# Kernel optimization log

Hardware: AMD Instinct MI355X
Metric: run time of the kernel (lower is better)

The kernel has to match this reference:

```python
import jax, jax.numpy as jnp
import numpy as np

IN_FEATURES = 3
CODE_NUM = 64
CODE_CHANNEL = 64
SHAPE_NUM = 1


def setup_inputs() -> dict:
    key = jax.random.key(0)
    k1, k2 = jax.random.split(key)
    coords = jax.random.uniform(k1, (8, 65536, IN_FEATURES), dtype=jnp.float32)  # in [0,1) subset of [-1,1]
    table_size = SHAPE_NUM * CODE_NUM ** IN_FEATURES
    # xavier_uniform for [C, N] matrix
    limit = float(np.sqrt(6.0 / (CODE_CHANNEL + table_size)))
    shape_code = jax.random.uniform(k2, (CODE_CHANNEL, table_size), dtype=jnp.float32,
                                    minval=-limit, maxval=limit)
    return {"coords": coords, "shape_code": shape_code, "idx": 0}


def reference(coords, shape_code, idx):
    D = IN_FEATURES
    # corner offset mask: [2^D, D] of {0,1}
    mask = jnp.stack(jnp.meshgrid(*([jnp.arange(2, dtype=jnp.float32)] * D), indexing="ij"), -1)
    mask = mask.reshape(-1, D)                                   # [8, 3]
    mul = jnp.asarray([CODE_NUM ** i for i in range(D)], dtype=jnp.int64)
    offset = jnp.asarray(idx, dtype=jnp.int64) * (CODE_NUM ** D)

    c = (coords + 1.0) * ((CODE_NUM - 1) / 2.0)                  # [B, P, 3] in [0, code_num-1]
    corners = jnp.floor(c)[..., None, :] + mask                  # [B, P, 8, 3]
    coordsf = c[..., None, :] - corners                          # [B, P, 8, 3]
    index = jnp.sum(corners.astype(jnp.int64) * mul, axis=-1) + offset  # [B, P, 8]
    weights = jnp.prod(1.0 - jnp.abs(coordsf), axis=-1)          # [B, P, 8]

    code = jnp.take(shape_code, index, axis=1)                   # [C, B, P, 8] gather
    out = jnp.einsum("cbpk,bpk->bpc", code, weights)             # weighted corner sum
    return out
```

## Files before the change

kernel.cpp:

```cpp
#include <hip/hip_runtime.h>


#define CODE_NUM 64
#define CODE_CHANNEL 64
#define TABLE (CODE_NUM * CODE_NUM * CODE_NUM)
#define NBINS 4096
#define SCAT_PTS 1024
#define SCAT_PPT 4
#define TBLOCKS (TABLE / 64)
#define LROW 68

typedef float f4_t __attribute__((ext_vector_type(4)));

__device__ __forceinline__ void nt_store_f4(float* p, float x, float y, float z, float w) {
    f4_t v = {x, y, z, w};
    __builtin_nontemporal_store(v, (f4_t*)p);
}

__global__ __launch_bounds__(256) void init_k(int* __restrict__ hist, int* __restrict__ bbox,
                                              int* __restrict__ done) {
    const int t = blockIdx.x * 256 + threadIdx.x;
    for (int i = t; i < NBINS; i += gridDim.x * 256) hist[i] = 0;
    if (t == 0) {
        bbox[0] = 0x7fffffff; bbox[1] = (int)0x80000000;
        bbox[2] = 0x7fffffff; bbox[3] = (int)0x80000000;
        done[0] = 0;
    }
}

__device__ __forceinline__ int cell_bin(float x, float y, float z,
                                        int& ix, int& iy, int& iz) {
    ix = (int)floorf((x + 1.0f) * ((CODE_NUM - 1) * 0.5f));
    iy = (int)floorf((y + 1.0f) * ((CODE_NUM - 1) * 0.5f));
    iz = (int)floorf((z + 1.0f) * ((CODE_NUM - 1) * 0.5f));
    const int cx = min(max(ix, 0), 63) >> 2;
    const int cy = min(max(iy, 0), 63) >> 2;
    const int cz = min(max(iz, 0), 63) >> 2;
    return cx | (cy << 4) | (cz << 8);
}

__global__ __launch_bounds__(256) void hist_scan_k(const float* __restrict__ coords, int npoints,
                                                   int* __restrict__ hist, int* __restrict__ bbox,
                                                   int* __restrict__ done,
                                                   int* __restrict__ cursor,
                                                   int* __restrict__ starts) {
    __shared__ int lh[NBINS];
    __shared__ int lb[4];
    __shared__ int lastflag;
    __shared__ int wbase[4];
    for (int i = threadIdx.x; i < NBINS; i += 256) lh[i] = 0;
    if (threadIdx.x == 0) {
        lb[0] = 0x7fffffff; lb[1] = (int)0x80000000;
        lb[2] = 0x7fffffff; lb[3] = (int)0x80000000;
        lastflag = 0;
    }
    __syncthreads();
    int ymin = 0x7fffffff, ymax = (int)0x80000000;
    int zmin = 0x7fffffff, zmax = (int)0x80000000;
    const int stride = gridDim.x * 256;
    for (int p = blockIdx.x * 256 + threadIdx.x; p < npoints; p += stride) {
        const float x = coords[p * 3 + 0];
        const float y = coords[p * 3 + 1];
        const float z = coords[p * 3 + 2];
        int ix, iy, iz;
        const int bin = cell_bin(x, y, z, ix, iy, iz);
        atomicAdd(&lh[bin], 1);
        ymin = min(ymin, iy); ymax = max(ymax, iy);
        zmin = min(zmin, iz); zmax = max(zmax, iz);
    }
    atomicMin(&lb[0], ymin); atomicMax(&lb[1], ymax);
    atomicMin(&lb[2], zmin); atomicMax(&lb[3], zmax);
    __syncthreads();
    for (int i = threadIdx.x; i < NBINS; i += 256) {
        const int c = lh[i];
        if (c) atomicAdd(&hist[i], c);
    }
    if (threadIdx.x == 0) {
        atomicMin(&bbox[0], lb[0]); atomicMax(&bbox[1], lb[1]);
        atomicMin(&bbox[2], lb[2]); atomicMax(&bbox[3], lb[3]);
    }
    __threadfence();
    __syncthreads();
    if (threadIdx.x == 0) {
        const int r = atomicAdd(done, 1);
        if (r == (int)gridDim.x - 1) lastflag = 1;
    }
    __syncthreads();
    if (!lastflag) return;

    const int t = threadIdx.x;
    int h[16];
    int s = 0;
#pragma unroll
    for (int j = 0; j < 16; ++j) {
        h[j] = atomicAdd(&hist[t * 16 + j], 0);
        s += h[j];
    }
    const int lane = t & 63, wv = t >> 6;
    int inc = s;
#pragma unroll
    for (int d = 1; d < 64; d <<= 1) {
        const int u = __shfl_up(inc, d, 64);
        if (lane >= d) inc += u;
    }
    if (lane == 63) wbase[wv] = inc;
    __syncthreads();
    int wex = 0;
#pragma unroll
    for (int w = 0; w < 4; ++w)
        if (w < wv) wex += wbase[w];
    int run = wex + (inc - s);
#pragma unroll
    for (int j = 0; j < 16; ++j) {
        cursor[t * 16 + j] = run;
        starts[t * 16 + j] = run;
        run += h[j];
    }
    if (t == 255) starts[NBINS] = npoints;
}

__global__ __launch_bounds__(256) void mid_fused_k(const float* __restrict__ src,
                                                   float* __restrict__ dst,
                                                   const int* __restrict__ bbox,
                                                   const float* __restrict__ coords, int npoints,
                                                   int* __restrict__ cursor,
                                                   float4* __restrict__ sorted) {
    __shared__ int smem[64 * 65];

    if (blockIdx.x < TBLOCKS) {
        const int t0 = blockIdx.x * 64;
        const int y = (t0 >> 6) & 63;
        const int z = t0 >> 12;
        if (y < bbox[0] || y > bbox[1] + 1 || z < bbox[2] || z > bbox[3] + 1) return;

        float* tile = (float*)smem;
        const int j = threadIdx.x;
#pragma unroll
        for (int i = 0; i < 4; ++i) {
            const int q = (i << 8) | j;
            const int c = q >> 4;
            const int tc4 = q & 15;
            const float4 v = *(const float4*)(src + (size_t)c * TABLE + t0 + (tc4 << 2));
            tile[((tc4 << 2) + 0) * 65 + c] = v.x;
            tile[((tc4 << 2) + 1) * 65 + c] = v.y;
            tile[((tc4 << 2) + 2) * 65 + c] = v.z;
            tile[((tc4 << 2) + 3) * 65 + c] = v.w;
        }
        __syncthreads();
#pragma unroll
        for (int i = 0; i < 4; ++i) {
            const int q = (i << 8) | j;
            const int t = q >> 4;
            const int c4 = q & 15;
            nt_store_f4(dst + (size_t)(t0 + t) * 64 + (c4 << 2),
                        tile[t * 65 + (c4 << 2) + 0],
                        tile[t * 65 + (c4 << 2) + 1],
                        tile[t * 65 + (c4 << 2) + 2],
                        tile[t * 65 + (c4 << 2) + 3]);
        }
    } else {
        int* lcount = smem;
        for (int i = threadIdx.x; i < NBINS; i += 256) lcount[i] = 0;
        __syncthreads();

        const int p0 = (int)(blockIdx.x - TBLOCKS) * SCAT_PTS;
        float px[SCAT_PPT], py[SCAT_PPT], pz[SCAT_PPT];
        int pbin[SCAT_PPT], prank[SCAT_PPT];

#pragma unroll
        for (int i = 0; i < SCAT_PPT; ++i) {
            const int p = p0 + (i << 8) + (int)threadIdx.x;
            pbin[i] = -1;
            if (p < npoints) {
                const float x = coords[p * 3 + 0];
                const float y = coords[p * 3 + 1];
                const float z = coords[p * 3 + 2];
                int ix, iy, iz;
                const int bin = cell_bin(x, y, z, ix, iy, iz);
                px[i] = x; py[i] = y; pz[i] = z;
                pbin[i] = bin;
                prank[i] = atomicAdd(&lcount[bin], 1);
            }
        }
        __syncthreads();

        for (int i = threadIdx.x; i < NBINS; i += 256) {
            const int c = lcount[i];
            if (c) lcount[i] = atomicAdd(&cursor[i], c);
        }
        __syncthreads();

#pragma unroll
        for (int i = 0; i < SCAT_PPT; ++i) {
            if (pbin[i] >= 0) {
                const int p = p0 + (i << 8) + (int)threadIdx.x;
                const int slot = lcount[pbin[i]] + prank[i];
                sorted[slot] = make_float4(px[i], py[i], pz[i], __int_as_float(p));
            }
        }
    }
}

__global__ __launch_bounds__(256) void interp_bin_k(const float4* __restrict__ sorted,
                                                    const float* __restrict__ table,
                                                    const int* __restrict__ starts,
                                                    float* __restrict__ out,
                                                    int npoints) {
    unsigned bid = blockIdx.x;
    bid = (bid & 7u) * (NBINS / 8) + (bid >> 3);
    const int s = starts[bid];
    const int e = starts[bid + 1];
    if (e <= s) return;

    const int x0 = (bid & 15) << 2;
    const int y0 = ((bid >> 4) & 15) << 2;
    const int z0 = (bid >> 8) << 2;

    __shared__ float lds[125 * LROW];

    const f4_t* tt4 = (const f4_t*)table;
    for (int i = threadIdx.x; i < 125 * 16; i += 256) {
        const int row = i >> 4, o = i & 15;
        const int dx = row % 5;
        const int seg = row / 5;
        const int dy = seg % 5, dz = seg / 5;
        const int cell = (z0 + dz) * (CODE_NUM * CODE_NUM) + (y0 + dy) * CODE_NUM + (x0 + dx);
        *(f4_t*)&lds[row * LROW + (o << 2)] = tt4[(size_t)cell * 16 + o];
    }
    __syncthreads();

    const int lane = threadIdx.x & 63;
    const int wv = threadIdx.x >> 6;
    const int sub = lane >> 4;
    const int cg = lane & 15;

    for (int p = s + wv * 4 + sub; p < e; p += 16) {
        const float4 s4 = sorted[p];
        const int op = __float_as_int(s4.w);

        const float sx = (s4.x + 1.0f) * ((CODE_NUM - 1) * 0.5f);
        const float sy = (s4.y + 1.0f) * ((CODE_NUM - 1) * 0.5f);
        const float sz = (s4.z + 1.0f) * ((CODE_NUM - 1) * 0.5f);
        const float fx = floorf(sx), fy = floorf(sy), fz = floorf(sz);
        const float rx = sx - fx, ry = sy - fy, rz = sz - fz;
        const int ix = (int)fx, iy = (int)fy, iz = (int)fz;
        const int r0 = ((iz - z0) * 5 + (iy - y0)) * 5 + (ix - x0);

        const float wx[2] = {1.0f - rx, rx};
        const float wy[2] = {1.0f - ry, ry};
        const float wz[2] = {1.0f - rz, rz};

        float4 acc = make_float4(0.f, 0.f, 0.f, 0.f);
#pragma unroll
        for (int k = 0; k < 8; ++k) {
            const int a = k & 1, b = (k >> 1) & 1, c = (k >> 2) & 1;
            const int row = r0 + a + 5 * b + 25 * c;
            const float w = wx[a] * wy[b] * wz[c];
            const float4 v = *(const float4*)&lds[row * LROW + (cg << 2)];
            acc.x = fmaf(w, v.x, acc.x);
            acc.y = fmaf(w, v.y, acc.y);
            acc.z = fmaf(w, v.z, acc.z);
            acc.w = fmaf(w, v.w, acc.w);
        }
        nt_store_f4(out + (size_t)op * CODE_CHANNEL + (cg << 2), acc.x, acc.y, acc.z, acc.w);
    }
}

__global__ __launch_bounds__(256) void transpose_k(const float* __restrict__ src,
                                                   float* __restrict__ dst) {
    __shared__ float tile[64 * 65];
    const int t0 = blockIdx.x * 64;
    const int j = threadIdx.x;
#pragma unroll
    for (int i = 0; i < 4; ++i) {
        const int q = (i << 8) | j;
        const int c = q >> 4;
        const int tc4 = q & 15;
        const float4 v = *(const float4*)(src + (size_t)c * TABLE + t0 + (tc4 << 2));
        tile[((tc4 << 2) + 0) * 65 + c] = v.x;
        tile[((tc4 << 2) + 1) * 65 + c] = v.y;
        tile[((tc4 << 2) + 2) * 65 + c] = v.z;
        tile[((tc4 << 2) + 3) * 65 + c] = v.w;
    }
    __syncthreads();
#pragma unroll
    for (int i = 0; i < 4; ++i) {
        const int q = (i << 8) | j;
        const int t = q >> 4;
        const int c4 = q & 15;
        float4 v;
        v.x = tile[t * 65 + (c4 << 2) + 0];
        v.y = tile[t * 65 + (c4 << 2) + 1];
        v.z = tile[t * 65 + (c4 << 2) + 2];
        v.w = tile[t * 65 + (c4 << 2) + 3];
        *(float4*)(dst + (size_t)(t0 + t) * 64 + (c4 << 2)) = v;
    }
}

__global__ __launch_bounds__(256) void interp4_k(const float* __restrict__ coords,
                                                 const float* __restrict__ table,
                                                 const int* __restrict__ idxp,
                                                 float* __restrict__ out,
                                                 int npoints) {
    const unsigned tid = blockIdx.x * 256u + threadIdx.x;
    const int lane = threadIdx.x & 63;
    const int sub = lane >> 4;
    const int cg = lane & 15;
    const int p = (int)((tid >> 6) * 4u + (unsigned)sub);
    if (p >= npoints) return;

    const int offset = idxp[0] * TABLE;
    const float sx = (coords[p * 3 + 0] + 1.0f) * ((CODE_NUM - 1) * 0.5f);
    const float sy = (coords[p * 3 + 1] + 1.0f) * ((CODE_NUM - 1) * 0.5f);
    const float sz = (coords[p * 3 + 2] + 1.0f) * ((CODE_NUM - 1) * 0.5f);
    const float fx = floorf(sx), fy = floorf(sy), fz = floorf(sz);
    const float rx = sx - fx, ry = sy - fy, rz = sz - fz;
    const int ix = (int)fx, iy = (int)fy, iz = (int)fz;
    const int base = offset + ix + iy * CODE_NUM + iz * (CODE_NUM * CODE_NUM);
    const float wx[2] = {1.0f - rx, rx};
    const float wy[2] = {1.0f - ry, ry};
    const float wz[2] = {1.0f - rz, rz};
    const char* tp = (const char*)table;
    const int cgoff = cg << 4;
    float4 acc = make_float4(0.f, 0.f, 0.f, 0.f);
#pragma unroll
    for (int k = 0; k < 8; ++k) {
        const int a = k & 1, b = (k >> 1) & 1, c = (k >> 2) & 1;
        const int idx = base + a + b * CODE_NUM + c * (CODE_NUM * CODE_NUM);
        const float w = wx[a] * wy[b] * wz[c];
        const float4 v = *(const float4*)(tp + ((size_t)(unsigned)(idx << 8) + cgoff));
        acc.x = fmaf(w, v.x, acc.x);
        acc.y = fmaf(w, v.y, acc.y);
        acc.z = fmaf(w, v.z, acc.z);
        acc.w = fmaf(w, v.w, acc.w);
    }
    *(float4*)(out + (size_t)p * CODE_CHANNEL + (cg << 2)) = acc;
}

__global__ __launch_bounds__(256) void interp_fallback_k(const float* __restrict__ coords,
                                                         const float* __restrict__ table,
                                                         const int* __restrict__ idxp,
                                                         float* __restrict__ out,
                                                         int npoints) {
    const int p = (int)((blockIdx.x * 256u + threadIdx.x) >> 6);
    const int lane = threadIdx.x & 63;
    if (p >= npoints) return;
    const int offset = idxp[0] * TABLE;
    const float sx = (coords[p * 3 + 0] + 1.0f) * ((CODE_NUM - 1) * 0.5f);
    const float sy = (coords[p * 3 + 1] + 1.0f) * ((CODE_NUM - 1) * 0.5f);
    const float sz = (coords[p * 3 + 2] + 1.0f) * ((CODE_NUM - 1) * 0.5f);
    const float fx = floorf(sx), fy = floorf(sy), fz = floorf(sz);
    const float rx = sx - fx, ry = sy - fy, rz = sz - fz;
    const int base = offset + (int)fx + (int)fy * CODE_NUM + (int)fz * (CODE_NUM * CODE_NUM);
    const float wx[2] = {1.0f - rx, rx};
    const float wy[2] = {1.0f - ry, ry};
    const float wz[2] = {1.0f - rz, rz};
    float acc = 0.0f;
#pragma unroll
    for (int k = 0; k < 8; ++k) {
        const int a = k & 1, b = (k >> 1) & 1, c = (k >> 2) & 1;
        const int idx = base + a + b * CODE_NUM + c * (CODE_NUM * CODE_NUM);
        acc = fmaf(wx[a] * wy[b] * wz[c], table[(size_t)lane * TABLE + idx], acc);
    }
    out[(size_t)p * CODE_CHANNEL + lane] = acc;
}

extern "C" void kernel_launch(void* const* d_in, const int* in_sizes, int n_in,
                              void* d_out, int out_size, void* d_ws, size_t ws_size,
                              hipStream_t stream) {
    const float* coords = (const float*)d_in[0];
    const float* code   = (const float*)d_in[1];
    const int*   idxp   = (const int*)d_in[2];
    float* out = (float*)d_out;

    const int npoints = in_sizes[0] / 3;
    const size_t tbytes = (size_t)TABLE * CODE_CHANNEL * sizeof(float);
    const size_t sbytes = (size_t)npoints * sizeof(float4);
    const size_t abytes = (size_t)(NBINS + NBINS + NBINS + 1 + 4 + 1 + 16) * sizeof(int);
    const size_t need = tbytes + sbytes + abytes;

    if (ws_size >= need) {
        char* w = (char*)d_ws;
        float*  tt     = (float*)w;
        float4* sorted = (float4*)(w + tbytes);
        int*    hist   = (int*)(w + tbytes + sbytes);
        int*    cursor = hist + NBINS;
        int*    starts = cursor + NBINS;
        int*    bbox   = starts + NBINS + 1;
        int*    done   = bbox + 4;

        const int nscat = (npoints + SCAT_PTS - 1) / SCAT_PTS;

        init_k<<<16, 256, 0, stream>>>(hist, bbox, done);
        hist_scan_k<<<128, 256, 0, stream>>>(coords, npoints, hist, bbox, done, cursor, starts);
        mid_fused_k<<<TBLOCKS + nscat, 256, 0, stream>>>(code, tt, bbox,
                                                         coords, npoints, cursor, sorted);
        interp_bin_k<<<NBINS, 256, 0, stream>>>(sorted, tt, starts, out, npoints);
    } else if (ws_size >= tbytes) {
        float* tt = (float*)d_ws;
        transpose_k<<<TABLE / 64, 256, 0, stream>>>(code, tt);
        interp4_k<<<(npoints + 15) / 16, 256, 0, stream>>>(coords, tt, idxp, out, npoints);
    } else {
        interp_fallback_k<<<(npoints + 3) / 4, 256, 0, stream>>>(coords, code, idxp, out, npoints);
    }
}
```

Baseline: 285.2 us.

## Split spatial bins into fixed-size point chunks for balanced interpolation blocks

The interpolation kernel used one block per spatial bin, so dense bins became long serial blocks while most of the 4096 blocks exited early. The scan kernel now emits a work list of (bin, start) items, each covering at most 256 sorted points, using an atomic counter. The interpolation kernel launches one block per item and bounds its range by the chunk end. This should spread work over more blocks and balance load across CUs, at the cost of reloading the bin's table neighbourhood into LDS once per chunk instead of once per bin.

```diff
diff --git a/kernel.cpp b/kernel.cpp
--- a/kernel.cpp
+++ b/kernel.cpp
@@ -9,6 +9,8 @@
 #define SCAT_PPT 4
 #define TBLOCKS (TABLE / 64)
 #define LROW 68
+#define CHUNK 256
+#define MAXITEMS 8192
 
 typedef float f4_t __attribute__((ext_vector_type(4)));
 
@@ -18,13 +20,14 @@
 }
 
 __global__ __launch_bounds__(256) void init_k(int* __restrict__ hist, int* __restrict__ bbox,
-                                              int* __restrict__ done) {
+                                              int* __restrict__ done, int* __restrict__ nitems) {
     const int t = blockIdx.x * 256 + threadIdx.x;
     for (int i = t; i < NBINS; i += gridDim.x * 256) hist[i] = 0;
     if (t == 0) {
         bbox[0] = 0x7fffffff; bbox[1] = (int)0x80000000;
         bbox[2] = 0x7fffffff; bbox[3] = (int)0x80000000;
         done[0] = 0;
+        nitems[0] = 0;
     }
 }
 
@@ -43,7 +46,9 @@
                                                    int* __restrict__ hist, int* __restrict__ bbox,
                                                    int* __restrict__ done,
                                                    int* __restrict__ cursor,
-                                                   int* __restrict__ starts) {
+                                                   int* __restrict__ starts,
+                                                   int* __restrict__ nitems,
+                                                   int2* __restrict__ items) {
     __shared__ int lh[NBINS];
     __shared__ int lb[4];
     __shared__ int lastflag;
@@ -112,9 +117,17 @@
     int run = wex + (inc - s);
 #pragma unroll
     for (int j = 0; j < 16; ++j) {
-        cursor[t * 16 + j] = run;
-        starts[t * 16 + j] = run;
-        run += h[j];
+        const int bin = t * 16 + j;
+        cursor[bin] = run;
+        starts[bin] = run;
+        const int c = h[j];
+        if (c > 0) {
+            const int nch = (c + CHUNK - 1) / CHUNK;
+            const int base = atomicAdd(nitems, nch);
+            for (int k = 0; k < nch; ++k)
+                items[base + k] = make_int2(bin, run + k * CHUNK);
+        }
+        run += c;
     }
     if (t == 255) starts[NBINS] = npoints;
 }
@@ -201,20 +214,27 @@
     }
 }
 
-__global__ __launch_bounds__(256) void interp_bin_k(const float4* __restrict__ sorted,
-                                                    const float* __restrict__ table,
-                                                    const int* __restrict__ starts,
-                                                    float* __restrict__ out,
-                                                    int npoints) {
+__global__ __launch_bounds__(256) void interp_chunk_k(const float4* __restrict__ sorted,
+                                                      const float* __restrict__ table,
+                                                      const int* __restrict__ starts,
+                                                      const int* __restrict__ nitems,
+                                                      const int2* __restrict__ items,
+                                                      float* __restrict__ out) {
     unsigned bid = blockIdx.x;
-    bid = (bid & 7u) * (NBINS / 8) + (bid >> 3);
-    const int s = starts[bid];
-    const int e = starts[bid + 1];
-    if (e <= s) return;
-
-    const int x0 = (bid & 15) << 2;
-    const int y0 = ((bid >> 4) & 15) << 2;
-    const int z0 = (bid >> 8) << 2;
+    const unsigned nb = gridDim.x;
+    if ((nb & 7u) == 0u) {
+        const unsigned c = nb >> 3;
+        bid = (bid & 7u) * c + (bid >> 3);
+    }
+    if ((int)bid >= nitems[0]) return;
+    const int2 it = items[bid];
+    const int bin = it.x;
+    const int s = it.y;
+    const int e = min(starts[bin + 1], s + CHUNK);
+
+    const int x0 = (bin & 15) << 2;
+    const int y0 = ((bin >> 4) & 15) << 2;
+    const int z0 = (bin >> 8) << 2;
 
     __shared__ float lds[125 * LROW];
 
@@ -376,7 +396,8 @@
     const int npoints = in_sizes[0] / 3;
     const size_t tbytes = (size_t)TABLE * CODE_CHANNEL * sizeof(float);
     const size_t sbytes = (size_t)npoints * sizeof(float4);
-    const size_t abytes = (size_t)(NBINS + NBINS + NBINS + 1 + 4 + 1 + 16) * sizeof(int);
+    const size_t abytes = (size_t)(3 * NBINS + 1 + 4 + 1 + 1 + 16) * sizeof(int)
+                        + (size_t)MAXITEMS * sizeof(int2);
     const size_t need = tbytes + sbytes + abytes;
 
     if (ws_size >= need) {
@@ -388,14 +409,18 @@
         int*    starts = cursor + NBINS;
         int*    bbox   = starts + NBINS + 1;
         int*    done   = bbox + 4;
+        int*    nitems = done + 1;
+        int2*   items  = (int2*)(nitems + 9);
 
         const int nscat = (npoints + SCAT_PTS - 1) / SCAT_PTS;
-
-        init_k<<<16, 256, 0, stream>>>(hist, bbox, done);
-        hist_scan_k<<<128, 256, 0, stream>>>(coords, npoints, hist, bbox, done, cursor, starts);
+        const int nint = NBINS + (npoints + CHUNK - 1) / CHUNK;
+
+        init_k<<<16, 256, 0, stream>>>(hist, bbox, done, nitems);
+        hist_scan_k<<<128, 256, 0, stream>>>(coords, npoints, hist, bbox, done,
+                                             cursor, starts, nitems, items);
         mid_fused_k<<<TBLOCKS + nscat, 256, 0, stream>>>(code, tt, bbox,
                                                          coords, npoints, cursor, sorted);
-        interp_bin_k<<<NBINS, 256, 0, stream>>>(sorted, tt, starts, out, npoints);
+        interp_chunk_k<<<nint, 256, 0, stream>>>(sorted, tt, starts, nitems, items, out);
     } else if (ws_size >= tbytes) {
         float* tt = (float*)d_ws;
         transpose_k<<<TABLE / 64, 256, 0, stream>>>(code, tt);
```

After: 323.1 us. 13.3% more time.
